# Kernel tuning notes

Measured on AMD Instinct MI355X. Metric: run time of the kernel, lower is better.

The kernel has to match this reference:

```python
import jax, jax.numpy as jnp
import numpy as np

N, B, H, D = 8, 4, 16, 64   # batch, beam, heads, head_dim
T, S, L = 16, 1024, 1024    # new tokens, prefix len, past len
E = H * D
SCALE = 1.0 / np.sqrt(D).astype(np.float32)


def setup_inputs() -> dict:
    key = jax.random.key(0)
    ks = jax.random.split(key, 10)
    wscale = 1.0 / np.sqrt(E).astype(np.float32)
    return {
        "hidden_states": jax.random.normal(ks[0], (N * B, T, E), jnp.float32),
        "attention_mask": jnp.zeros((N * B, 1, 1, S + L + T), jnp.float32),
        "rel_pos": jax.random.normal(ks[1], (N * B, H, T, S + L + T), jnp.float32) * 0.1,
        "past_prefix_key": jax.random.normal(ks[2], (N, H, S, D), jnp.float32),
        "past_prefix_value": jax.random.normal(ks[3], (N, H, S, D), jnp.float32),
        "past_key": jax.random.normal(ks[4], (N * B, H, L, D), jnp.float32),
        "past_value": jax.random.normal(ks[5], (N * B, H, L, D), jnp.float32),
        "Wq": jax.random.normal(ks[6], (E, E), jnp.float32) * wscale,
        "bq": jnp.zeros((E,), jnp.float32),
        "Wk": jax.random.normal(ks[7], (E, E), jnp.float32) * wscale,
        "bk": jnp.zeros((E,), jnp.float32),
        "Wv": jax.random.normal(ks[8], (E, E), jnp.float32) * wscale,
        "bv": jnp.zeros((E,), jnp.float32),
    }


def _heads(x):
    # (NB, T, E) -> (NB, H, T, D)
    nb, t, _ = x.shape
    return x.reshape(nb, t, H, D).transpose(0, 2, 1, 3)


def reference(hidden_states, attention_mask, rel_pos, past_prefix_key,
              past_prefix_value, past_key, past_value, Wq, bq, Wk, bk, Wv, bv):
    q = _heads(hidden_states @ Wq.T + bq)   # (NB,H,T,D)
    k = _heads(hidden_states @ Wk.T + bk)
    v = _heads(hidden_states @ Wv.T + bv)

    # prefix scores: batch-shared prefix KV, per-beam queries
    q5 = q.reshape(N, B, H, T, D)
    prefix_scores = jnp.einsum('bxhtd,bhsd->bxhts', q5, past_prefix_key)
    prefix_scores = prefix_scores.reshape(N * B, H, T, S) * SCALE

    key_layer = jnp.concatenate([past_key, k], axis=2)      # (NB,H,L+T,D)
    value_layer = jnp.concatenate([past_value, v], axis=2)
    scores = jnp.einsum('bhtd,bhsd->bhts', q, key_layer) * SCALE

    scores = jnp.concatenate([prefix_scores, scores], axis=-1)  # (NB,H,T,S+L+T)
    scores = scores + rel_pos + attention_mask
    probs = jax.nn.softmax(scores, axis=-1)

    prefix_probs = probs[..., :S]
    rest_probs = probs[..., S:]

    prefix_ctx = jnp.einsum('bxhts,bhsd->bxhtd',
                            prefix_probs.reshape(N, B, H, T, S),
                            past_prefix_value).reshape(N * B, H, T, D)
    ctx = prefix_ctx + jnp.einsum('bhts,bhsd->bhtd', rest_probs, value_layer)

    # (NB,H,T,D) -> (NB,T,E)
    return ctx.transpose(0, 2, 1, 3).reshape(N * B, T, E)
```

## Files before the change

### kernel.cpp

```cpp
#include <hip/hip_runtime.h>

#define NH 16
#define NT 16
#define DD 64
#define SS 1024
#define LL 1024
#define TOTK 2064
#define EE 1024
#define NWAVE 8

typedef __attribute__((ext_vector_type(8))) short bf16x8;
typedef __attribute__((ext_vector_type(4))) float f32x4;

__device__ __forceinline__ unsigned short f2bf(float x) {
  union { float f; unsigned u; } v; v.f = x;
  unsigned r = v.u + 0x7fffu + ((v.u >> 16) & 1u);
  return (unsigned short)(r >> 16);
}
__device__ __forceinline__ unsigned pkbf(float a, float b) {
  unsigned r;
  asm("v_cvt_pk_bf16_f32 %0, %1, %2" : "=v"(r) : "v"(a), "v"(b));
  return r;
}
union BF8 { unsigned u[4]; bf16x8 v; };

__device__ __forceinline__ void dma16(const void* g, void* l) {
  __builtin_amdgcn_global_load_lds(
      (const __attribute__((address_space(1))) unsigned int*)g,
      (__attribute__((address_space(3))) unsigned int*)l, 16, 0, 0);
}

__global__ __launch_bounds__(256)
void proj_kernel(const float* __restrict__ hidden,
                 const float* __restrict__ Wq, const float* __restrict__ bq,
                 const float* __restrict__ Wk, const float* __restrict__ bk,
                 const float* __restrict__ Wv, const float* __restrict__ bv,
                 unsigned short* __restrict__ qws,
                 float* __restrict__ kws, float* __restrict__ vws)
{
  __shared__ alignas(16) unsigned short As[64][72];
  __shared__ alignas(16) unsigned short Bs[64][72];
  const int mtile = blockIdx.x;
  const int ntile = blockIdx.y;
  const int mat = ntile >> 4;
  const int h = ntile & 15;
  const float* Wm = (mat == 0) ? Wq : (mat == 1 ? Wk : Wv);
  const float* bm = (mat == 0) ? bq : (mat == 1 ? bk : bv);
  const int tid = threadIdx.x;
  const int lane = tid & 63, w = tid >> 6;
  const int lr = lane & 15, lg = lane >> 4;
  const int m0 = mtile * 64;

  const f32x4 fz = {0.f, 0.f, 0.f, 0.f};
  f32x4 acc[4];
  #pragma unroll
  for (int j = 0; j < 4; ++j) acc[j] = fz;

  const int srow = tid >> 4, sc4 = tid & 15;
  float4 Ar[4], Br[4];
  #pragma unroll
  for (int it = 0; it < 4; ++it) {
    Ar[it] = *(const float4*)(hidden + (m0 + srow + it * 16) * EE + sc4 * 4);
    Br[it] = *(const float4*)(Wm + (h * 64 + srow + it * 16) * EE + sc4 * 4);
  }

  for (int k0 = 0; k0 < EE; k0 += 64) {
    __syncthreads();
    #pragma unroll
    for (int it = 0; it < 4; ++it) {
      int row = srow + it * 16;
      float4 a = Ar[it], b = Br[it];
      *(uint2*)(&As[row][sc4 * 4]) = make_uint2(pkbf(a.x, a.y), pkbf(a.z, a.w));
      *(uint2*)(&Bs[row][sc4 * 4]) = make_uint2(pkbf(b.x, b.y), pkbf(b.z, b.w));
    }
    __syncthreads();
    int kn = k0 + 64;
    if (kn < EE) {
      #pragma unroll
      for (int it = 0; it < 4; ++it) {
        Ar[it] = *(const float4*)(hidden + (m0 + srow + it * 16) * EE + kn + sc4 * 4);
        Br[it] = *(const float4*)(Wm + (h * 64 + srow + it * 16) * EE + kn + sc4 * 4);
      }
    }
    #pragma unroll
    for (int hh = 0; hh < 2; ++hh) {
      bf16x8 a = *(const bf16x8*)(&As[w * 16 + lr][hh * 32 + lg * 8]);
      #pragma unroll
      for (int dt = 0; dt < 4; ++dt) {
        bf16x8 b = *(const bf16x8*)(&Bs[dt * 16 + lr][hh * 32 + lg * 8]);
        acc[dt] = __builtin_amdgcn_mfma_f32_16x16x32_bf16(a, b, acc[dt], 0, 0, 0);
      }
    }
  }

  #pragma unroll
  for (int dt = 0; dt < 4; ++dt)
    #pragma unroll
    for (int r = 0; r < 4; ++r) {
      int Mrow = m0 + w * 16 + lg * 4 + r;
      int nb = Mrow >> 4, t = Mrow & 15;
      int d = dt * 16 + lr;
      float val = acc[dt][r] + bm[h * 64 + d];
      int oi = ((nb * NH + h) * NT + t) * DD + d;
      if (mat == 0) qws[oi] = f2bf(val);
      else if (mat == 1) kws[oi] = val;
      else vws[oi] = val;
    }
}

__global__ __launch_bounds__(512, 2)
void prefix_attn_kernel(const float* __restrict__ mask, const float* __restrict__ rel,
                        const float* __restrict__ ppk, const float* __restrict__ ppv,
                        const unsigned short* __restrict__ qws,
                        float* __restrict__ pfn, float* __restrict__ pfd)
{
  __shared__ __align__(16) float SB[2 * 128 * 64];
  __shared__ __align__(16) unsigned short Pb[NWAVE][16][40];

  const int bidx = blockIdx.x;
  const int h = bidx & 15;
  const int sn = bidx >> 4;
  const int nn = sn & 7;
  const int s = sn >> 3;
  const int tid = threadIdx.x;
  const int lane = tid & 63, w = tid >> 6;
  const int lr = lane & 15, lg = lane >> 4;
  const int key0 = s * 512;

  bf16x8 aq[4][2];
  #pragma unroll
  for (int b = 0; b < 4; ++b) {
    const unsigned short* qb = qws + (((nn * 4 + b) * NH + h) * NT) * DD;
    aq[b][0] = *(const bf16x8*)(qb + lr * DD + lg * 8);
    aq[b][1] = *(const bf16x8*)(qb + lr * DD + lg * 8 + 32);
  }

  const f32x4 fz = {0.f, 0.f, 0.f, 0.f};
  f32x4 ctx[4][4];
  float ls[4][4];
  #pragma unroll
  for (int b = 0; b < 4; ++b)
    #pragma unroll
    for (int j = 0; j < 4; ++j) { ctx[b][j] = fz; ls[b][j] = 0.f; }

  auto kstage = [&](int c, int buf) {
    const float* ks = ppk + ((nn * NH + h) * SS + key0 + c * 128) * DD;
    float* Kb = SB + buf * 128 * 64;
    #pragma unroll
    for (int q = 0; q < 4; ++q) {
      int Lrow = w * 16 + q * 4 + (lane >> 4);
      int colb = (lane & 15) * 16;
      int scolb = colb ^ ((Lrow & 7) << 4);
      dma16((const char*)ks + Lrow * 256 + scolb, Kb + (w * 16 + q * 4) * 64);
    }
  };

  kstage(0, 0);
  kstage(1, 1);

  #pragma unroll
  for (int p = 0; p < 2; ++p) {
    const int cA = 2 * p;
    const int kbA = key0 + cA * 128 + w * 16;

    const float* vs = ppv + ((nn * NH + h) * SS + key0 + cA * 128) * DD;
    float vraw[32];
    #pragma unroll
    for (int dt = 0; dt < 4; ++dt)
      #pragma unroll
      for (int e = 0; e < 8; ++e) {
        int kslot = lg * 8 + e;
        int j = (kslot >> 4) * 128 + w * 16 + (kslot & 15);
        vraw[dt * 8 + e] = vs[j * DD + dt * 16 + lr];
      }

    __builtin_amdgcn_sched_barrier(0);
    asm volatile("s_waitcnt vmcnt(32)" ::: "memory");
    __builtin_amdgcn_sched_barrier(0);

    float rr[4][2][4]; float mk[4][2];
    #pragma unroll
    for (int b = 0; b < 4; ++b) {
      const float* relb = rel + (((nn * 4 + b) * NH + h) * NT) * TOTK;
      const float* mb = mask + (nn * 4 + b) * TOTK;
      #pragma unroll
      for (int r = 0; r < 4; ++r) {
        rr[b][0][r] = relb[(lg * 4 + r) * TOTK + kbA + lr];
        rr[b][1][r] = relb[(lg * 4 + r) * TOTK + kbA + 128 + lr];
      }
      mk[b][0] = mb[kbA + lr];
      mk[b][1] = mb[kbA + 128 + lr];
    }

    bf16x8 kbf[2][2];
    #pragma unroll
    for (int sub = 0; sub < 2; ++sub) {
      const char* Kb = (const char*)(SB + sub * 128 * 64);
      #pragma unroll
      for (int hh = 0; hh < 2; ++hh) {
        int c0 = (hh * 128 + lg * 32) ^ ((lr & 7) << 4);
        int c1 = (hh * 128 + lg * 32 + 16) ^ ((lr & 7) << 4);
        float4 v0 = *(const float4*)(Kb + (w * 16 + lr) * 256 + c0);
        float4 v1 = *(const float4*)(Kb + (w * 16 + lr) * 256 + c1);
        BF8 o;
        o.u[0] = pkbf(v0.x, v0.y); o.u[1] = pkbf(v0.z, v0.w);
        o.u[2] = pkbf(v1.x, v1.y); o.u[3] = pkbf(v1.z, v1.w);
        kbf[sub][hh] = o.v;
      }
    }

    __builtin_amdgcn_sched_barrier(0);
    if (p == 0) { kstage(2, 0); kstage(3, 1); }
    __builtin_amdgcn_sched_barrier(0);

    bf16x8 vb[4];
    #pragma unroll
    for (int dt = 0; dt < 4; ++dt) {
      BF8 o;
      #pragma unroll
      for (int q = 0; q < 4; ++q)
        o.u[q] = pkbf(vraw[dt * 8 + q * 2], vraw[dt * 8 + q * 2 + 1]);
      vb[dt] = o.v;
    }

    #pragma unroll
    for (int b = 0; b < 4; ++b) {
      f32x4 sA = fz, sB = fz;
      sA = __builtin_amdgcn_mfma_f32_16x16x32_bf16(aq[b][0], kbf[0][0], sA, 0, 0, 0);
      sA = __builtin_amdgcn_mfma_f32_16x16x32_bf16(aq[b][1], kbf[0][1], sA, 0, 0, 0);
      sB = __builtin_amdgcn_mfma_f32_16x16x32_bf16(aq[b][0], kbf[1][0], sB, 0, 0, 0);
      sB = __builtin_amdgcn_mfma_f32_16x16x32_bf16(aq[b][1], kbf[1][1], sB, 0, 0, 0);
      #pragma unroll
      for (int r = 0; r < 4; ++r) {
        float pA = __expf(sA[r] * 0.125f + rr[b][0][r] + mk[b][0]);
        float pB = __expf(sB[r] * 0.125f + rr[b][1][r] + mk[b][1]);
        ls[b][r] += pA + pB;
        Pb[w][lg * 4 + r][lr] = f2bf(pA);
        Pb[w][lg * 4 + r][16 + lr] = f2bf(pB);
      }
      bf16x8 pa = *(const bf16x8*)(&Pb[w][lr][lg * 8]);
      #pragma unroll
      for (int dt = 0; dt < 4; ++dt)
        ctx[b][dt] = __builtin_amdgcn_mfma_f32_16x16x32_bf16(pa, vb[dt], ctx[b][dt], 0, 0, 0);
    }
  }

  #pragma unroll
  for (int b = 0; b < 4; ++b)
    #pragma unroll
    for (int r = 0; r < 4; ++r) {
      #pragma unroll
      for (int o = 8; o >= 1; o >>= 1) ls[b][r] += __shfl_xor(ls[b][r], o, 16);
    }

  float* mgc = SB;
  float* mgl = SB + NWAVE * 16 * 64;
  for (int b = 0; b < 4; ++b) {
    __syncthreads();
    #pragma unroll
    for (int dt = 0; dt < 4; ++dt)
      #pragma unroll
      for (int r = 0; r < 4; ++r)
        mgc[(w * 16 + lg * 4 + r) * 64 + dt * 16 + lr] = ctx[b][dt][r];
    if (lr == 0) {
      #pragma unroll
      for (int r = 0; r < 4; ++r) mgl[w * 16 + lg * 4 + r] = ls[b][r];
    }
    __syncthreads();
    #pragma unroll
    for (int i = 0; i < 2; ++i) {
      int idx = i * 512 + tid;
      int t = idx >> 6, d = idx & 63;
      float num = 0.f, den = 0.f;
      #pragma unroll
      for (int ww = 0; ww < NWAVE; ++ww) {
        den += mgl[ww * 16 + t];
        num += mgc[(ww * 16 + t) * 64 + d];
      }
      pfn[((sn * 16 + h) * 4 + b) * 1024 + t * 64 + d] = num;
      if (d == 0) pfd[((sn * 16 + h) * 4 + b) * 16 + t] = den;
    }
  }
}

__global__ __launch_bounds__(512, 2)
void past_attn_kernel(const float* __restrict__ mask, const float* __restrict__ rel,
                      const float* __restrict__ pk, const float* __restrict__ pv,
                      const unsigned short* __restrict__ qws,
                      const float* __restrict__ kws, const float* __restrict__ vws,
                      const float* __restrict__ pfn, const float* __restrict__ pfd,
                      float* __restrict__ out)
{
  __shared__ __align__(16) float SB[2 * 128 * 64];
  __shared__ __align__(16) unsigned short Pb[NWAVE][16][40];

  const int wg = blockIdx.x;
  const int nb = wg >> 4, h = wg & 15;
  const int tid = threadIdx.x;
  const int lane = tid & 63, w = tid >> 6;
  const int lr = lane & 15, lg = lane >> 4;

  const unsigned short* qbase = qws + ((nb * NH + h) * NT) * DD;
  bf16x8 aq0 = *(const bf16x8*)(qbase + lr * DD + lg * 8);
  bf16x8 aq1 = *(const bf16x8*)(qbase + lr * DD + lg * 8 + 32);

  const float* relbase = rel + ((nb * NH + h) * NT) * TOTK;
  const float* mbase = mask + nb * TOTK;

  const f32x4 fz = {0.f, 0.f, 0.f, 0.f};
  f32x4 ctx[4];
  float ls[4];
  #pragma unroll
  for (int dt = 0; dt < 4; ++dt) ctx[dt] = fz;
  #pragma unroll
  for (int r = 0; r < 4; ++r) ls[r] = 0.f;

  auto kstage = [&](int c, int buf) {
    const float* ks = (c < 8) ? pk + ((nb * NH + h) * LL + c * 128) * DD
                              : kws + ((nb * NH + h) * NT) * DD;
    float* Kb = SB + buf * 128 * 64;
    #pragma unroll
    for (int q = 0; q < 4; ++q) {
      int Lrow = w * 16 + q * 4 + (lane >> 4);
      int colb = (lane & 15) * 16;
      int scolb = colb ^ ((Lrow & 7) << 4);
      int srow = (c == 8) ? (Lrow & 15) : Lrow;
      dma16((const char*)ks + srow * 256 + scolb, Kb + (w * 16 + q * 4) * 64);
    }
  };

  auto qk_sub = [&](const float* Kb, const float rr[4], float mv, int sub) {
    bf16x8 kbf[2];
    #pragma unroll
    for (int hh = 0; hh < 2; ++hh) {
      int c0 = (hh * 128 + lg * 32) ^ ((lr & 7) << 4);
      int c1 = (hh * 128 + lg * 32 + 16) ^ ((lr & 7) << 4);
      float4 v0 = *(const float4*)((const char*)Kb + (w * 16 + lr) * 256 + c0);
      float4 v1 = *(const float4*)((const char*)Kb + (w * 16 + lr) * 256 + c1);
      BF8 o;
      o.u[0] = pkbf(v0.x, v0.y); o.u[1] = pkbf(v0.z, v0.w);
      o.u[2] = pkbf(v1.x, v1.y); o.u[3] = pkbf(v1.z, v1.w);
      kbf[hh] = o.v;
    }
    f32x4 s = fz;
    s = __builtin_amdgcn_mfma_f32_16x16x32_bf16(aq0, kbf[0], s, 0, 0, 0);
    s = __builtin_amdgcn_mfma_f32_16x16x32_bf16(aq1, kbf[1], s, 0, 0, 0);
    #pragma unroll
    for (int r = 0; r < 4; ++r) {
      float p = __expf(s[r] * 0.125f + rr[r] + mv);
      ls[r] += p;
      Pb[w][lg * 4 + r][sub * 16 + lr] = f2bf(p);
    }
  };

  auto rel_load = [&](int cA, float (&rA)[4], float (&rB)[4], float& mA, float& mB) {
    int kbA = SS + cA * 128 + w * 16, kbB = kbA + 128;
    #pragma unroll
    for (int r = 0; r < 4; ++r) {
      rA[r] = relbase[(lg * 4 + r) * TOTK + kbA + lr];
      rB[r] = relbase[(lg * 4 + r) * TOTK + kbB + lr];
    }
    mA = mbase[kbA + lr];
    mB = mbase[kbB + lr];
  };

  auto pair_iter = [&](int p, float (&rA)[4], float (&rB)[4], float& mA, float& mB,
                       float (&rAn)[4], float (&rBn)[4], float& mAn, float& mBn) {
    const int cA = 2 * p;

    __builtin_amdgcn_sched_barrier(0);
    asm volatile("s_waitcnt vmcnt(10)" ::: "memory");
    __builtin_amdgcn_sched_barrier(0);

    const float* vs = pv + ((nb * NH + h) * LL + cA * 128) * DD;
    float vraw[32];
    #pragma unroll
    for (int dt = 0; dt < 4; ++dt)
      #pragma unroll
      for (int e = 0; e < 8; ++e) {
        int kslot = lg * 8 + e;
        int j = (kslot >> 4) * 128 + w * 16 + (kslot & 15);
        vraw[dt * 8 + e] = vs[j * DD + dt * 16 + lr];
      }
    __builtin_amdgcn_sched_barrier(0);

    qk_sub(SB, rA, mA, 0);
    qk_sub(SB + 128 * 64, rB, mB, 1);

    __builtin_amdgcn_sched_barrier(0);
    if (p < 3) {
      kstage(cA + 2, 0);
      kstage(cA + 3, 1);
      rel_load(cA + 2, rAn, rBn, mAn, mBn);
    } else {
      kstage(8, 0);
    }
    __builtin_amdgcn_sched_barrier(0);

    bf16x8 pa = *(const bf16x8*)(&Pb[w][lr][lg * 8]);
    #pragma unroll
    for (int dt = 0; dt < 4; ++dt) {
      BF8 o;
      #pragma unroll
      for (int q = 0; q < 4; ++q)
        o.u[q] = pkbf(vraw[dt * 8 + q * 2], vraw[dt * 8 + q * 2 + 1]);
      ctx[dt] = __builtin_amdgcn_mfma_f32_16x16x32_bf16(pa, o.v, ctx[dt], 0, 0, 0);
    }
  };

  kstage(0, 0);
  kstage(1, 1);
  float ra0[4], rb0[4], ma0, mb0, ra1[4], rb1[4], ma1, mb1;
  rel_load(0, ra0, rb0, ma0, mb0);
  ma1 = mb1 = 0.f; ra1[0]=ra1[1]=ra1[2]=ra1[3]=0.f; rb1[0]=rb1[1]=rb1[2]=rb1[3]=0.f;

  for (int p = 0; p < 4; p += 2) {
    pair_iter(p,     ra0, rb0, ma0, mb0, ra1, rb1, ma1, mb1);
    pair_iter(p + 1, ra1, rb1, ma1, mb1, ra0, rb0, ma0, mb0);
  }

  if (w == 0) {
    #pragma unroll
    for (int r = 0; r < 4; ++r) Pb[0][lg * 4 + r][16 + lr] = 0;
    const float* vs = vws + ((nb * NH + h) * NT) * DD;
    float vraw[32];
    #pragma unroll
    for (int dt = 0; dt < 4; ++dt)
      #pragma unroll
      for (int e = 0; e < 8; ++e) {
        int kslot = lg * 8 + e;
        vraw[dt * 8 + e] = (kslot < 16) ? vs[kslot * DD + dt * 16 + lr] : 0.f;
      }
    float rrT[4];
    #pragma unroll
    for (int r = 0; r < 4; ++r)
      rrT[r] = relbase[(lg * 4 + r) * TOTK + 2048 + lr];
    float mvT = mbase[2048 + lr];

    __builtin_amdgcn_sched_barrier(0);
    asm volatile("s_waitcnt vmcnt(0)" ::: "memory");
    __builtin_amdgcn_sched_barrier(0);

    qk_sub(SB, rrT, mvT, 0);

    bf16x8 pa = *(const bf16x8*)(&Pb[0][lr][lg * 8]);
    #pragma unroll
    for (int dt = 0; dt < 4; ++dt) {
      BF8 o;
      #pragma unroll
      for (int q = 0; q < 4; ++q)
        o.u[q] = pkbf(vraw[dt * 8 + q * 2], vraw[dt * 8 + q * 2 + 1]);
      ctx[dt] = __builtin_amdgcn_mfma_f32_16x16x32_bf16(pa, o.v, ctx[dt], 0, 0, 0);
    }
  }

  #pragma unroll
  for (int r = 0; r < 4; ++r) {
    #pragma unroll
    for (int o = 8; o >= 1; o >>= 1) ls[r] += __shfl_xor(ls[r], o, 16);
  }

  __syncthreads();
  float* mgc = SB;
  float* mgl = SB + NWAVE * 16 * 64;
  #pragma unroll
  for (int dt = 0; dt < 4; ++dt)
    #pragma unroll
    for (int r = 0; r < 4; ++r)
      mgc[(w * 16 + lg * 4 + r) * 64 + dt * 16 + lr] = ctx[dt][r];
  if (lr == 0) {
    #pragma unroll
    for (int r = 0; r < 4; ++r) mgl[w * 16 + lg * 4 + r] = ls[r];
  }
  __syncthreads();
  const int n = nb >> 2, b = nb & 3;
  #pragma unroll
  for (int i = 0; i < 2; ++i) {
    int idx = i * 512 + tid;
    int t = idx >> 6, d = idx & 63;
    float num = 0.f, den = 0.f;
    #pragma unroll
    for (int ww = 0; ww < NWAVE; ++ww) {
      den += mgl[ww * 16 + t];
      num += mgc[(ww * 16 + t) * 64 + d];
    }
    #pragma unroll
    for (int sp = 0; sp < 2; ++sp) {
      int pbase = (((sp * 8 + n) * 16 + h) * 4 + b);
      num += pfn[pbase * 1024 + t * 64 + d];
      den += pfd[pbase * 16 + t];
    }
    out[((nb * NT + t) * NH + h) * DD + d] = num / den;
  }
}

extern "C" void kernel_launch(void* const* d_in, const int* in_sizes, int n_in,
                              void* d_out, int out_size, void* d_ws, size_t ws_size,
                              hipStream_t stream) {
  const float* hidden = (const float*)d_in[0];
  const float* mask   = (const float*)d_in[1];
  const float* rel    = (const float*)d_in[2];
  const float* ppk    = (const float*)d_in[3];
  const float* ppv    = (const float*)d_in[4];
  const float* pk     = (const float*)d_in[5];
  const float* pv     = (const float*)d_in[6];
  const float* Wq     = (const float*)d_in[7];
  const float* bq     = (const float*)d_in[8];
  const float* Wk     = (const float*)d_in[9];
  const float* bk     = (const float*)d_in[10];
  const float* Wv     = (const float*)d_in[11];
  const float* bv     = (const float*)d_in[12];
  float* out = (float*)d_out;

  unsigned short* qws = (unsigned short*)d_ws;
  float* kws = (float*)((char*)d_ws + (1u << 20));
  float* vws = (float*)((char*)d_ws + 3u * (1u << 20));
  float* pfn = (float*)((char*)d_ws + 5u * (1u << 20));
  float* pfd = (float*)((char*)d_ws + 9u * (1u << 20));

  proj_kernel<<<dim3(8, 48), 256, 0, stream>>>(hidden, Wq, bq, Wk, bk, Wv, bv,
                                               qws, kws, vws);
  prefix_attn_kernel<<<dim3(256), 512, 0, stream>>>(mask, rel, ppk, ppv,
                                                    qws, pfn, pfd);
  past_attn_kernel<<<dim3(512), 512, 0, stream>>>(mask, rel, pk, pv,
                                                  qws, kws, vws, pfn, pfd, out);
}
```

Measured before the change: 110.0 us.

## Merge prefix and past attention into one launch with separate merge kernel

Combines the prefix-attention and past-attention kernels into a single 768-block launch, with blocks 0-511 doing past attention and the rest doing prefix attention, so both run concurrently instead of back to back. Past-attention partial numerators and denominators now go to workspace, and a small merge kernel adds them to the prefix partials and normalizes. The partial vmcnt waits are replaced by full drains (vmcnt(0)), which removes some load/compute overlap. The extra kernel and the workspace round trip add overhead.

```diff
diff --git a/kernel.cpp b/kernel.cpp
--- a/kernel.cpp
+++ b/kernel.cpp
@@ -29,6 +29,10 @@
       (const __attribute__((address_space(1))) unsigned int*)g,
       (__attribute__((address_space(3))) unsigned int*)l, 16, 0, 0);
 }
+#define DRAIN() do { \
+    asm volatile("s_waitcnt vmcnt(0)" ::: "memory"); \
+    __builtin_amdgcn_sched_barrier(0); \
+  } while (0)
 
 __global__ __launch_bounds__(256)
 void proj_kernel(const float* __restrict__ hidden,
@@ -109,162 +113,189 @@
 }
 
 __global__ __launch_bounds__(512, 2)
-void prefix_attn_kernel(const float* __restrict__ mask, const float* __restrict__ rel,
-                        const float* __restrict__ ppk, const float* __restrict__ ppv,
-                        const unsigned short* __restrict__ qws,
-                        float* __restrict__ pfn, float* __restrict__ pfd)
+void attn_fat_kernel(const float* __restrict__ mask, const float* __restrict__ rel,
+                     const float* __restrict__ ppk, const float* __restrict__ ppv,
+                     const float* __restrict__ pk, const float* __restrict__ pv,
+                     const unsigned short* __restrict__ qws,
+                     const float* __restrict__ kws, const float* __restrict__ vws,
+                     float* __restrict__ pfn, float* __restrict__ pfd,
+                     float* __restrict__ pn, float* __restrict__ pd)
 {
   __shared__ __align__(16) float SB[2 * 128 * 64];
   __shared__ __align__(16) unsigned short Pb[NWAVE][16][40];
 
-  const int bidx = blockIdx.x;
-  const int h = bidx & 15;
-  const int sn = bidx >> 4;
-  const int nn = sn & 7;
-  const int s = sn >> 3;
   const int tid = threadIdx.x;
   const int lane = tid & 63, w = tid >> 6;
   const int lr = lane & 15, lg = lane >> 4;
-  const int key0 = s * 512;
-
-  bf16x8 aq[4][2];
-  #pragma unroll
-  for (int b = 0; b < 4; ++b) {
-    const unsigned short* qb = qws + (((nn * 4 + b) * NH + h) * NT) * DD;
-    aq[b][0] = *(const bf16x8*)(qb + lr * DD + lg * 8);
-    aq[b][1] = *(const bf16x8*)(qb + lr * DD + lg * 8 + 32);
-  }
-
   const f32x4 fz = {0.f, 0.f, 0.f, 0.f};
-  f32x4 ctx[4][4];
-  float ls[4][4];
-  #pragma unroll
-  for (int b = 0; b < 4; ++b)
-    #pragma unroll
-    for (int j = 0; j < 4; ++j) { ctx[b][j] = fz; ls[b][j] = 0.f; }
-
-  auto kstage = [&](int c, int buf) {
-    const float* ks = ppk + ((nn * NH + h) * SS + key0 + c * 128) * DD;
-    float* Kb = SB + buf * 128 * 64;
-    #pragma unroll
-    for (int q = 0; q < 4; ++q) {
-      int Lrow = w * 16 + q * 4 + (lane >> 4);
-      int colb = (lane & 15) * 16;
-      int scolb = colb ^ ((Lrow & 7) << 4);
-      dma16((const char*)ks + Lrow * 256 + scolb, Kb + (w * 16 + q * 4) * 64);
-    }
-  };
-
-  kstage(0, 0);
-  kstage(1, 1);
-
-  #pragma unroll
-  for (int p = 0; p < 2; ++p) {
-    const int cA = 2 * p;
-    const int kbA = key0 + cA * 128 + w * 16;
-
-    const float* vs = ppv + ((nn * NH + h) * SS + key0 + cA * 128) * DD;
-    float vraw[32];
-    #pragma unroll
-    for (int dt = 0; dt < 4; ++dt)
-      #pragma unroll
-      for (int e = 0; e < 8; ++e) {
-        int kslot = lg * 8 + e;
-        int j = (kslot >> 4) * 128 + w * 16 + (kslot & 15);
-        vraw[dt * 8 + e] = vs[j * DD + dt * 16 + lr];
-      }
-
-    __builtin_amdgcn_sched_barrier(0);
-    asm volatile("s_waitcnt vmcnt(32)" ::: "memory");
-    __builtin_amdgcn_sched_barrier(0);
-
-    float rr[4][2][4]; float mk[4][2];
-    #pragma unroll
-    for (int b = 0; b < 4; ++b) {
-      const float* relb = rel + (((nn * 4 + b) * NH + h) * NT) * TOTK;
-      const float* mb = mask + (nn * 4 + b) * TOTK;
-      #pragma unroll
-      for (int r = 0; r < 4; ++r) {
-        rr[b][0][r] = relb[(lg * 4 + r) * TOTK + kbA + lr];
-        rr[b][1][r] = relb[(lg * 4 + r) * TOTK + kbA + 128 + lr];
-      }
-      mk[b][0] = mb[kbA + lr];
-      mk[b][1] = mb[kbA + 128 + lr];
-    }
-
-    bf16x8 kbf[2][2];
-    #pragma unroll
-    for (int sub = 0; sub < 2; ++sub) {
-      const char* Kb = (const char*)(SB + sub * 128 * 64);
+
+  if (blockIdx.x < 512) {
+    const int wg = blockIdx.x;
+    const int nb = wg >> 4, h = wg & 15;
+
+    const unsigned short* qbase = qws + ((nb * NH + h) * NT) * DD;
+    bf16x8 aq0 = *(const bf16x8*)(qbase + lr * DD + lg * 8);
+    bf16x8 aq1 = *(const bf16x8*)(qbase + lr * DD + lg * 8 + 32);
+
+    const float* relbase = rel + ((nb * NH + h) * NT) * TOTK;
+    const float* mbase = mask + nb * TOTK;
+
+    f32x4 ctx[4];
+    float ls[4];
+    #pragma unroll
+    for (int dt = 0; dt < 4; ++dt) ctx[dt] = fz;
+    #pragma unroll
+    for (int r = 0; r < 4; ++r) ls[r] = 0.f;
+
+    auto kstage = [&](int c, int buf) {
+      const float* ks = (c < 8) ? pk + ((nb * NH + h) * LL + c * 128) * DD
+                                : kws + ((nb * NH + h) * NT) * DD;
+      float* Kb = SB + buf * 128 * 64;
+      #pragma unroll
+      for (int q = 0; q < 4; ++q) {
+        int Lrow = w * 16 + q * 4 + (lane >> 4);
+        int colb = (lane & 15) * 16;
+        int scolb = colb ^ ((Lrow & 7) << 4);
+        int srow = (c == 8) ? (Lrow & 15) : Lrow;
+        dma16((const char*)ks + srow * 256 + scolb, Kb + (w * 16 + q * 4) * 64);
+      }
+    };
+
+    auto qk_sub = [&](const float* Kb, const float rr[4], float mv, int sub) {
+      bf16x8 kbf[2];
       #pragma unroll
       for (int hh = 0; hh < 2; ++hh) {
         int c0 = (hh * 128 + lg * 32) ^ ((lr & 7) << 4);
         int c1 = (hh * 128 + lg * 32 + 16) ^ ((lr & 7) << 4);
-        float4 v0 = *(const float4*)(Kb + (w * 16 + lr) * 256 + c0);
-        float4 v1 = *(const float4*)(Kb + (w * 16 + lr) * 256 + c1);
+        float4 v0 = *(const float4*)((const char*)Kb + (w * 16 + lr) * 256 + c0);
+        float4 v1 = *(const float4*)((const char*)Kb + (w * 16 + lr) * 256 + c1);
         BF8 o;
         o.u[0] = pkbf(v0.x, v0.y); o.u[1] = pkbf(v0.z, v0.w);
         o.u[2] = pkbf(v1.x, v1.y); o.u[3] = pkbf(v1.z, v1.w);
-        kbf[sub][hh] = o.v;
-      }
-    }
-
-    __builtin_amdgcn_sched_barrier(0);
-    if (p == 0) { kstage(2, 0); kstage(3, 1); }
-    __builtin_amdgcn_sched_barrier(0);
-
-    bf16x8 vb[4];
-    #pragma unroll
-    for (int dt = 0; dt < 4; ++dt) {
-      BF8 o;
-      #pragma unroll
-      for (int q = 0; q < 4; ++q)
-        o.u[q] = pkbf(vraw[dt * 8 + q * 2], vraw[dt * 8 + q * 2 + 1]);
-      vb[dt] = o.v;
-    }
-
-    #pragma unroll
-    for (int b = 0; b < 4; ++b) {
-      f32x4 sA = fz, sB = fz;
-      sA = __builtin_amdgcn_mfma_f32_16x16x32_bf16(aq[b][0], kbf[0][0], sA, 0, 0, 0);
-      sA = __builtin_amdgcn_mfma_f32_16x16x32_bf16(aq[b][1], kbf[0][1], sA, 0, 0, 0);
-      sB = __builtin_amdgcn_mfma_f32_16x16x32_bf16(aq[b][0], kbf[1][0], sB, 0, 0, 0);
-      sB = __builtin_amdgcn_mfma_f32_16x16x32_bf16(aq[b][1], kbf[1][1], sB, 0, 0, 0);
+        kbf[hh] = o.v;
+      }
+      f32x4 s = fz;
+      s = __builtin_amdgcn_mfma_f32_16x16x32_bf16(aq0, kbf[0], s, 0, 0, 0);
+      s = __builtin_amdgcn_mfma_f32_16x16x32_bf16(aq1, kbf[1], s, 0, 0, 0);
       #pragma unroll
       for (int r = 0; r < 4; ++r) {
-        float pA = __expf(sA[r] * 0.125f + rr[b][0][r] + mk[b][0]);
-        float pB = __expf(sB[r] * 0.125f + rr[b][1][r] + mk[b][1]);
-        ls[b][r] += pA + pB;
-        Pb[w][lg * 4 + r][lr] = f2bf(pA);
-        Pb[w][lg * 4 + r][16 + lr] = f2bf(pB);
-      }
+        float p = __expf(s[r] * 0.125f + rr[r] + mv);
+        ls[r] += p;
+        Pb[w][lg * 4 + r][sub * 16 + lr] = f2bf(p);
+      }
+    };
+
+    auto rel_load = [&](int cA, float (&rA)[4], float (&rB)[4], float& mA, float& mB) {
+      int kbA = SS + cA * 128 + w * 16, kbB = kbA + 128;
+      #pragma unroll
+      for (int r = 0; r < 4; ++r) {
+        rA[r] = relbase[(lg * 4 + r) * TOTK + kbA + lr];
+        rB[r] = relbase[(lg * 4 + r) * TOTK + kbB + lr];
+      }
+      mA = mbase[kbA + lr];
+      mB = mbase[kbB + lr];
+    };
+
+    auto pair_iter = [&](int p, float (&rA)[4], float (&rB)[4], float& mA, float& mB,
+                         float (&rAn)[4], float (&rBn)[4], float& mAn, float& mBn) {
+      const int cA = 2 * p;
+
+      DRAIN();
+
+      const float* vs = pv + ((nb * NH + h) * LL + cA * 128) * DD;
+      float vraw[32];
+      #pragma unroll
+      for (int dt = 0; dt < 4; ++dt)
+        #pragma unroll
+        for (int e = 0; e < 8; ++e) {
+          int kslot = lg * 8 + e;
+          int j = (kslot >> 4) * 128 + w * 16 + (kslot & 15);
+          vraw[dt * 8 + e] = vs[j * DD + dt * 16 + lr];
+        }
+
+      qk_sub(SB, rA, mA, 0);
+      qk_sub(SB + 128 * 64, rB, mB, 1);
+
+      if (p < 3) {
+        kstage(cA + 2, 0);
+        kstage(cA + 3, 1);
+        rel_load(cA + 2, rAn, rBn, mAn, mBn);
+      } else {
+        kstage(8, 0);
+      }
+
       bf16x8 pa = *(const bf16x8*)(&Pb[w][lr][lg * 8]);
       #pragma unroll
+      for (int dt = 0; dt < 4; ++dt) {
+        BF8 o;
+        #pragma unroll
+        for (int q = 0; q < 4; ++q)
+          o.u[q] = pkbf(vraw[dt * 8 + q * 2], vraw[dt * 8 + q * 2 + 1]);
+        ctx[dt] = __builtin_amdgcn_mfma_f32_16x16x32_bf16(pa, o.v, ctx[dt], 0, 0, 0);
+      }
+    };
+
+    kstage(0, 0);
+    kstage(1, 1);
+    float ra0[4], rb0[4], ma0, mb0, ra1[4], rb1[4], ma1, mb1;
+    rel_load(0, ra0, rb0, ma0, mb0);
+    ma1 = mb1 = 0.f; ra1[0]=ra1[1]=ra1[2]=ra1[3]=0.f; rb1[0]=rb1[1]=rb1[2]=rb1[3]=0.f;
+
+    for (int p = 0; p < 4; p += 2) {
+      pair_iter(p,     ra0, rb0, ma0, mb0, ra1, rb1, ma1, mb1);
+      pair_iter(p + 1, ra1, rb1, ma1, mb1, ra0, rb0, ma0, mb0);
+    }
+
+    if (w == 0) {
+      #pragma unroll
+      for (int r = 0; r < 4; ++r) Pb[0][lg * 4 + r][16 + lr] = 0;
+      const float* vs = vws + ((nb * NH + h) * NT) * DD;
+      float vraw[32];
+      #pragma unroll
       for (int dt = 0; dt < 4; ++dt)
-        ctx[b][dt] = __builtin_amdgcn_mfma_f32_16x16x32_bf16(pa, vb[dt], ctx[b][dt], 0, 0, 0);
-    }
-  }
-
-  #pragma unroll
-  for (int b = 0; b < 4; ++b)
+        #pragma unroll
+        for (int e = 0; e < 8; ++e) {
+          int kslot = lg * 8 + e;
+          vraw[dt * 8 + e] = (kslot < 16) ? vs[kslot * DD + dt * 16 + lr] : 0.f;
+        }
+      float rrT[4];
+      #pragma unroll
+      for (int r = 0; r < 4; ++r)
+        rrT[r] = relbase[(lg * 4 + r) * TOTK + 2048 + lr];
+      float mvT = mbase[2048 + lr];
+
+      DRAIN();
+
+      qk_sub(SB, rrT, mvT, 0);
+
+      bf16x8 pa = *(const bf16x8*)(&Pb[0][lr][lg * 8]);
+      #pragma unroll
+      for (int dt = 0; dt < 4; ++dt) {
+        BF8 o;
+        #pragma unroll
+        for (int q = 0; q < 4; ++q)
+          o.u[q] = pkbf(vraw[dt * 8 + q * 2], vraw[dt * 8 + q * 2 + 1]);
+        ctx[dt] = __builtin_amdgcn_mfma_f32_16x16x32_bf16(pa, o.v, ctx[dt], 0, 0, 0);
+      }
+    }
+
     #pragma unroll
     for (int r = 0; r < 4; ++r) {
       #pragma unroll
-      for (int o = 8; o >= 1; o >>= 1) ls[b][r] += __shfl_xor(ls[b][r], o, 16);
-    }
-
-  float* mgc = SB;
-  float* mgl = SB + NWAVE * 16 * 64;
-  for (int b = 0; b < 4; ++b) {
+      for (int o = 8; o >= 1; o >>= 1) ls[r] += __shfl_xor(ls[r], o, 16);
+    }
+
     __syncthreads();
+    float* mgc = SB;
+    float* mgl = SB + NWAVE * 16 * 64;
     #pragma unroll
     for (int dt = 0; dt < 4; ++dt)
       #pragma unroll
       for (int r = 0; r < 4; ++r)
-        mgc[(w * 16 + lg * 4 + r) * 64 + dt * 16 + lr] = ctx[b][dt][r];
+        mgc[(w * 16 + lg * 4 + r) * 64 + dt * 16 + lr] = ctx[dt][r];
     if (lr == 0) {
       #pragma unroll
-      for (int r = 0; r < 4; ++r) mgl[w * 16 + lg * 4 + r] = ls[b][r];
+      for (int r = 0; r < 4; ++r) mgl[w * 16 + lg * 4 + r] = ls[r];
     }
     __syncthreads();
     #pragma unroll
@@ -277,213 +308,182 @@
         den += mgl[ww * 16 + t];
         num += mgc[(ww * 16 + t) * 64 + d];
       }
-      pfn[((sn * 16 + h) * 4 + b) * 1024 + t * 64 + d] = num;
-      if (d == 0) pfd[((sn * 16 + h) * 4 + b) * 16 + t] = den;
+      pn[(wg * 16 + t) * 64 + d] = num;
+      if (d == 0) pd[wg * 16 + t] = den;
+    }
+  } else {
+    const int bidx = blockIdx.x - 512;
+    const int h = bidx & 15;
+    const int sn = bidx >> 4;
+    const int nn = sn & 7;
+    const int s = sn >> 3;
+    const int key0 = s * 512;
+
+    bf16x8 aq[4][2];
+    #pragma unroll
+    for (int b = 0; b < 4; ++b) {
+      const unsigned short* qb = qws + (((nn * 4 + b) * NH + h) * NT) * DD;
+      aq[b][0] = *(const bf16x8*)(qb + lr * DD + lg * 8);
+      aq[b][1] = *(const bf16x8*)(qb + lr * DD + lg * 8 + 32);
+    }
+
+    f32x4 ctx[4][4];
+    float ls[4][4];
+    #pragma unroll
+    for (int b = 0; b < 4; ++b)
+      #pragma unroll
+      for (int j = 0; j < 4; ++j) { ctx[b][j] = fz; ls[b][j] = 0.f; }
+
+    auto kstage = [&](int c, int buf) {
+      const float* ks = ppk + ((nn * NH + h) * SS + key0 + c * 128) * DD;
+      float* Kb = SB + buf * 128 * 64;
+      #pragma unroll
+      for (int q = 0; q < 4; ++q) {
+        int Lrow = w * 16 + q * 4 + (lane >> 4);
+        int colb = (lane & 15) * 16;
+        int scolb = colb ^ ((Lrow & 7) << 4);
+        dma16((const char*)ks + Lrow * 256 + scolb, Kb + (w * 16 + q * 4) * 64);
+      }
+    };
+
+    kstage(0, 0);
+    kstage(1, 1);
+
+    for (int p = 0; p < 2; ++p) {
+      const int cA = 2 * p;
+      const int kbA = key0 + cA * 128 + w * 16;
+
+      DRAIN();
+
+      const float* vs = ppv + ((nn * NH + h) * SS + key0 + cA * 128) * DD;
+      float vraw[32];
+      #pragma unroll
+      for (int dt = 0; dt < 4; ++dt)
+        #pragma unroll
+        for (int e = 0; e < 8; ++e) {
+          int kslot = lg * 8 + e;
+          int j = (kslot >> 4) * 128 + w * 16 + (kslot & 15);
+          vraw[dt * 8 + e] = vs[j * DD + dt * 16 + lr];
+        }
+      float rr[4][2][4]; float mk[4][2];
+      #pragma unroll
+      for (int b = 0; b < 4; ++b) {
+        const float* relb = rel + (((nn * 4 + b) * NH + h) * NT) * TOTK;
+        const float* mb = mask + (nn * 4 + b) * TOTK;
+        #pragma unroll
+        for (int r = 0; r < 4; ++r) {
+          rr[b][0][r] = relb[(lg * 4 + r) * TOTK + kbA + lr];
+          rr[b][1][r] = relb[(lg * 4 + r) * TOTK + kbA + 128 + lr];
+        }
+        mk[b][0] = mb[kbA + lr];
+        mk[b][1] = mb[kbA + 128 + lr];
+      }
+
+      bf16x8 kbf[2][2];
+      #pragma unroll
+      for (int sub = 0; sub < 2; ++sub) {
+        const char* Kb = (const char*)(SB + sub * 128 * 64);
+        #pragma unroll
+        for (int hh = 0; hh < 2; ++hh) {
+          int c0 = (hh * 128 + lg * 32) ^ ((lr & 7) << 4);
+          int c1 = (hh * 128 + lg * 32 + 16) ^ ((lr & 7) << 4);
+          float4 v0 = *(const float4*)(Kb + (w * 16 + lr) * 256 + c0);
+          float4 v1 = *(const float4*)(Kb + (w * 16 + lr) * 256 + c1);
+          BF8 o;
+          o.u[0] = pkbf(v0.x, v0.y); o.u[1] = pkbf(v0.z, v0.w);
+          o.u[2] = pkbf(v1.x, v1.y); o.u[3] = pkbf(v1.z, v1.w);
+          kbf[sub][hh] = o.v;
+        }
+      }
+
+      if (p == 0) { kstage(2, 0); kstage(3, 1); }
+
+      bf16x8 vb[4];
+      #pragma unroll
+      for (int dt = 0; dt < 4; ++dt) {
+        BF8 o;
+        #pragma unroll
+        for (int q = 0; q < 4; ++q)
+          o.u[q] = pkbf(vraw[dt * 8 + q * 2], vraw[dt * 8 + q * 2 + 1]);
+        vb[dt] = o.v;
+      }
+
+      #pragma unroll
+      for (int b = 0; b < 4; ++b) {
+        f32x4 sA = fz, sB = fz;
+        sA = __builtin_amdgcn_mfma_f32_16x16x32_bf16(aq[b][0], kbf[0][0], sA, 0, 0, 0);
+        sA = __builtin_amdgcn_mfma_f32_16x16x32_bf16(aq[b][1], kbf[0][1], sA, 0, 0, 0);
+        sB = __builtin_amdgcn_mfma_f32_16x16x32_bf16(aq[b][0], kbf[1][0], sB, 0, 0, 0);
+        sB = __builtin_amdgcn_mfma_f32_16x16x32_bf16(aq[b][1], kbf[1][1], sB, 0, 0, 0);
+        #pragma unroll
+        for (int r = 0; r < 4; ++r) {
+          float pA = __expf(sA[r] * 0.125f + rr[b][0][r] + mk[b][0]);
+          float pB = __expf(sB[r] * 0.125f + rr[b][1][r] + mk[b][1]);
+          ls[b][r] += pA + pB;
+          Pb[w][lg * 4 + r][lr] = f2bf(pA);
+          Pb[w][lg * 4 + r][16 + lr] = f2bf(pB);
+        }
+        bf16x8 pa = *(const bf16x8*)(&Pb[w][lr][lg * 8]);
+        #pragma unroll
+        for (int dt = 0; dt < 4; ++dt)
+          ctx[b][dt] = __builtin_amdgcn_mfma_f32_16x16x32_bf16(pa, vb[dt], ctx[b][dt], 0, 0, 0);
+      }
+    }
+
+    #pragma unroll
+    for (int b = 0; b < 4; ++b)
+      #pragma unroll
+      for (int r = 0; r < 4; ++r) {
+        #pragma unroll
+        for (int o = 8; o >= 1; o >>= 1) ls[b][r] += __shfl_xor(ls[b][r], o, 16);
+      }
+
+    float* mgc = SB;
+    float* mgl = SB + NWAVE * 16 * 64;
+    for (int b = 0; b < 4; ++b) {
+      __syncthreads();
+      #pragma unroll
+      for (int dt = 0; dt < 4; ++dt)
+        #pragma unroll
+        for (int r = 0; r < 4; ++r)
+          mgc[(w * 16 + lg * 4 + r) * 64 + dt * 16 + lr] = ctx[b][dt][r];
+      if (lr == 0) {
+        #pragma unroll
+        for (int r = 0; r < 4; ++r) mgl[w * 16 + lg * 4 + r] = ls[b][r];
+      }
+      __syncthreads();
+      #pragma unroll
+      for (int i = 0; i < 2; ++i) {
+        int idx = i * 512 + tid;
+        int t = idx >> 6, d = idx & 63;
+        float num = 0.f, den = 0.f;
+        #pragma unroll
+        for (int ww = 0; ww < NWAVE; ++ww) {
+          den += mgl[ww * 16 + t];
+          num += mgc[(ww * 16 + t) * 64 + d];
+        }
+        pfn[((sn * 16 + h) * 4 + b) * 1024 + t * 64 + d] = num;
+        if (d == 0) pfd[((sn * 16 + h) * 4 + b) * 16 + t] = den;
+      }
     }
   }
 }
 
-__global__ __launch_bounds__(512, 2)
-void past_attn_kernel(const float* __restrict__ mask, const float* __restrict__ rel,
-                      const float* __restrict__ pk, const float* __restrict__ pv,
-                      const unsigned short* __restrict__ qws,
-                      const float* __restrict__ kws, const float* __restrict__ vws,
-                      const float* __restrict__ pfn, const float* __restrict__ pfd,
-                      float* __restrict__ out)
+__global__ __launch_bounds__(256)
+void merge_kernel(const float* __restrict__ pfn, const float* __restrict__ pfd,
+                  const float* __restrict__ pn, const float* __restrict__ pd,
+                  float* __restrict__ out)
 {
-  __shared__ __align__(16) float SB[2 * 128 * 64];
-  __shared__ __align__(16) unsigned short Pb[NWAVE][16][40];
-
   const int wg = blockIdx.x;
   const int nb = wg >> 4, h = wg & 15;
+  const int n = nb >> 2, b = nb & 3;
   const int tid = threadIdx.x;
-  const int lane = tid & 63, w = tid >> 6;
-  const int lr = lane & 15, lg = lane >> 4;
-
-  const unsigned short* qbase = qws + ((nb * NH + h) * NT) * DD;
-  bf16x8 aq0 = *(const bf16x8*)(qbase + lr * DD + lg * 8);
-  bf16x8 aq1 = *(const bf16x8*)(qbase + lr * DD + lg * 8 + 32);
-
-  const float* relbase = rel + ((nb * NH + h) * NT) * TOTK;
-  const float* mbase = mask + nb * TOTK;
-
-  const f32x4 fz = {0.f, 0.f, 0.f, 0.f};
-  f32x4 ctx[4];
-  float ls[4];
   #pragma unroll
-  for (int dt = 0; dt < 4; ++dt) ctx[dt] = fz;
-  #pragma unroll
-  for (int r = 0; r < 4; ++r) ls[r] = 0.f;
-
-  auto kstage = [&](int c, int buf) {
-    const float* ks = (c < 8) ? pk + ((nb * NH + h) * LL + c * 128) * DD
-                              : kws + ((nb * NH + h) * NT) * DD;
-    float* Kb = SB + buf * 128 * 64;
-    #pragma unroll
-    for (int q = 0; q < 4; ++q) {
-      int Lrow = w * 16 + q * 4 + (lane >> 4);
-      int colb = (lane & 15) * 16;
-      int scolb = colb ^ ((Lrow & 7) << 4);
-      int srow = (c == 8) ? (Lrow & 15) : Lrow;
-      dma16((const char*)ks + srow * 256 + scolb, Kb + (w * 16 + q * 4) * 64);
-    }
-  };
-
-  auto qk_sub = [&](const float* Kb, const float rr[4], float mv, int sub) {
-    bf16x8 kbf[2];
-    #pragma unroll
-    for (int hh = 0; hh < 2; ++hh) {
-      int c0 = (hh * 128 + lg * 32) ^ ((lr & 7) << 4);
-      int c1 = (hh * 128 + lg * 32 + 16) ^ ((lr & 7) << 4);
-      float4 v0 = *(const float4*)((const char*)Kb + (w * 16 + lr) * 256 + c0);
-      float4 v1 = *(const float4*)((const char*)Kb + (w * 16 + lr) * 256 + c1);
-      BF8 o;
-      o.u[0] = pkbf(v0.x, v0.y); o.u[1] = pkbf(v0.z, v0.w);
-      o.u[2] = pkbf(v1.x, v1.y); o.u[3] = pkbf(v1.z, v1.w);
-      kbf[hh] = o.v;
-    }
-    f32x4 s = fz;
-    s = __builtin_amdgcn_mfma_f32_16x16x32_bf16(aq0, kbf[0], s, 0, 0, 0);
-    s = __builtin_amdgcn_mfma_f32_16x16x32_bf16(aq1, kbf[1], s, 0, 0, 0);
-    #pragma unroll
-    for (int r = 0; r < 4; ++r) {
-      float p = __expf(s[r] * 0.125f + rr[r] + mv);
-      ls[r] += p;
-      Pb[w][lg * 4 + r][sub * 16 + lr] = f2bf(p);
-    }
-  };
-
-  auto rel_load = [&](int cA, float (&rA)[4], float (&rB)[4], float& mA, float& mB) {
-    int kbA = SS + cA * 128 + w * 16, kbB = kbA + 128;
-    #pragma unroll
-    for (int r = 0; r < 4; ++r) {
-      rA[r] = relbase[(lg * 4 + r) * TOTK + kbA + lr];
-      rB[r] = relbase[(lg * 4 + r) * TOTK + kbB + lr];
-    }
-    mA = mbase[kbA + lr];
-    mB = mbase[kbB + lr];
-  };
-
-  auto pair_iter = [&](int p, float (&rA)[4], float (&rB)[4], float& mA, float& mB,
-                       float (&rAn)[4], float (&rBn)[4], float& mAn, float& mBn) {
-    const int cA = 2 * p;
-
-    __builtin_amdgcn_sched_barrier(0);
-    asm volatile("s_waitcnt vmcnt(10)" ::: "memory");
-    __builtin_amdgcn_sched_barrier(0);
-
-    const float* vs = pv + ((nb * NH + h) * LL + cA * 128) * DD;
-    float vraw[32];
-    #pragma unroll
-    for (int dt = 0; dt < 4; ++dt)
-      #pragma unroll
-      for (int e = 0; e < 8; ++e) {
-        int kslot = lg * 8 + e;
-        int j = (kslot >> 4) * 128 + w * 16 + (kslot & 15);
-        vraw[dt * 8 + e] = vs[j * DD + dt * 16 + lr];
-      }
-    __builtin_amdgcn_sched_barrier(0);
-
-    qk_sub(SB, rA, mA, 0);
-    qk_sub(SB + 128 * 64, rB, mB, 1);
-
-    __builtin_amdgcn_sched_barrier(0);
-    if (p < 3) {
-      kstage(cA + 2, 0);
-      kstage(cA + 3, 1);
-      rel_load(cA + 2, rAn, rBn, mAn, mBn);
-    } else {
-      kstage(8, 0);
-    }
-    __builtin_amdgcn_sched_barrier(0);
-
-    bf16x8 pa = *(const bf16x8*)(&Pb[w][lr][lg * 8]);
-    #pragma unroll
-    for (int dt = 0; dt < 4; ++dt) {
-      BF8 o;
-      #pragma unroll
-      for (int q = 0; q < 4; ++q)
-        o.u[q] = pkbf(vraw[dt * 8 + q * 2], vraw[dt * 8 + q * 2 + 1]);
-      ctx[dt] = __builtin_amdgcn_mfma_f32_16x16x32_bf16(pa, o.v, ctx[dt], 0, 0, 0);
-    }
-  };
-
-  kstage(0, 0);
-  kstage(1, 1);
-  float ra0[4], rb0[4], ma0, mb0, ra1[4], rb1[4], ma1, mb1;
-  rel_load(0, ra0, rb0, ma0, mb0);
-  ma1 = mb1 = 0.f; ra1[0]=ra1[1]=ra1[2]=ra1[3]=0.f; rb1[0]=rb1[1]=rb1[2]=rb1[3]=0.f;
-
-  for (int p = 0; p < 4; p += 2) {
-    pair_iter(p,     ra0, rb0, ma0, mb0, ra1, rb1, ma1, mb1);
-    pair_iter(p + 1, ra1, rb1, ma1, mb1, ra0, rb0, ma0, mb0);
-  }
-
-  if (w == 0) {
-    #pragma unroll
-    for (int r = 0; r < 4; ++r) Pb[0][lg * 4 + r][16 + lr] = 0;
-    const float* vs = vws + ((nb * NH + h) * NT) * DD;
-    float vraw[32];
-    #pragma unroll
-    for (int dt = 0; dt < 4; ++dt)
-      #pragma unroll
-      for (int e = 0; e < 8; ++e) {
-        int kslot = lg * 8 + e;
-        vraw[dt * 8 + e] = (kslot < 16) ? vs[kslot * DD + dt * 16 + lr] : 0.f;
-      }
-    float rrT[4];
-    #pragma unroll
-    for (int r = 0; r < 4; ++r)
-      rrT[r] = relbase[(lg * 4 + r) * TOTK + 2048 + lr];
-    float mvT = mbase[2048 + lr];
-
-    __builtin_amdgcn_sched_barrier(0);
-    asm volatile("s_waitcnt vmcnt(0)" ::: "memory");
-    __builtin_amdgcn_sched_barrier(0);
-
-    qk_sub(SB, rrT, mvT, 0);
-
-    bf16x8 pa = *(const bf16x8*)(&Pb[0][lr][lg * 8]);
-    #pragma unroll
-    for (int dt = 0; dt < 4; ++dt) {
-      BF8 o;
-      #pragma unroll
-      for (int q = 0; q < 4; ++q)
-        o.u[q] = pkbf(vraw[dt * 8 + q * 2], vraw[dt * 8 + q * 2 + 1]);
-      ctx[dt] = __builtin_amdgcn_mfma_f32_16x16x32_bf16(pa, o.v, ctx[dt], 0, 0, 0);
-    }
-  }
-
-  #pragma unroll
-  for (int r = 0; r < 4; ++r) {
-    #pragma unroll
-    for (int o = 8; o >= 1; o >>= 1) ls[r] += __shfl_xor(ls[r], o, 16);
-  }
-
-  __syncthreads();
-  float* mgc = SB;
-  float* mgl = SB + NWAVE * 16 * 64;
-  #pragma unroll
-  for (int dt = 0; dt < 4; ++dt)
-    #pragma unroll
-    for (int r = 0; r < 4; ++r)
-      mgc[(w * 16 + lg * 4 + r) * 64 + dt * 16 + lr] = ctx[dt][r];
-  if (lr == 0) {
-    #pragma unroll
-    for (int r = 0; r < 4; ++r) mgl[w * 16 + lg * 4 + r] = ls[r];
-  }
-  __syncthreads();
-  const int n = nb >> 2, b = nb & 3;
-  #pragma unroll
-  for (int i = 0; i < 2; ++i) {
-    int idx = i * 512 + tid;
+  for (int i = 0; i < 4; ++i) {
+    int idx = i * 256 + tid;
     int t = idx >> 6, d = idx & 63;
-    float num = 0.f, den = 0.f;
-    #pragma unroll
-    for (int ww = 0; ww < NWAVE; ++ww) {
-      den += mgl[ww * 16 + t];
-      num += mgc[(ww * 16 + t) * 64 + d];
-    }
+    float num = pn[(wg * 16 + t) * 64 + d];
+    float den = pd[wg * 16 + t];
     #pragma unroll
     for (int sp = 0; sp < 2; ++sp) {
       int pbase = (((sp * 8 + n) * 16 + h) * 4 + b);
@@ -513,15 +513,16 @@
   float* out = (float*)d_out;
 
   unsigned short* qws = (unsigned short*)d_ws;
-  float* kws = (float*)((char*)d_ws + (1u << 20));
+  float* kws = (float*)((char*)d_ws + 1u * (1u << 20));
   float* vws = (float*)((char*)d_ws + 3u * (1u << 20));
   float* pfn = (float*)((char*)d_ws + 5u * (1u << 20));
   float* pfd = (float*)((char*)d_ws + 9u * (1u << 20));
+  float* pn  = (float*)((char*)d_ws + 10u * (1u << 20));
+  float* pd  = (float*)((char*)d_ws + 12u * (1u << 20));
 
   proj_kernel<<<dim3(8, 48), 256, 0, stream>>>(hidden, Wq, bq, Wk, bk, Wv, bv,
                                                qws, kws, vws);
-  prefix_attn_kernel<<<dim3(256), 512, 0, stream>>>(mask, rel, ppk, ppv,
-                                                    qws, pfn, pfd);
-  past_attn_kernel<<<dim3(512), 512, 0, stream>>>(mask, rel, pk, pv,
-                                                  qws, kws, vws, pfn, pfd, out);
-}
+  attn_fat_kernel<<<dim3(768), 512, 0, stream>>>(mask, rel, ppk, ppv, pk, pv,
+                                                 qws, kws, vws, pfn, pfd, pn, pd);
+  merge_kernel<<<dim3(512), 256, 0, stream>>>(pfn, pfd, pn, pd, out);
+}
```

Measured after the change: 114.1 us. 3.7% more time.
